# Optimization experiments

Measured on AMD Instinct MI355X. Metric: run time of the kernel, lower is better.

Reference implementation:

```python
import jax, jax.numpy as jnp
import numpy as np

D_MODEL = 1024
N_HEADS = 16
D_K = D_MODEL // N_HEADS  # 64
D_FF = 2688
THETA = 10000.0
EPS = 1e-5
B, S = 2, 2048


def _rmsnorm(x, w):
    xf = x.astype(jnp.float32)
    ms = jnp.mean(xf * xf, axis=-1, keepdims=True)
    return (xf * w * jax.lax.rsqrt(ms + EPS)).astype(x.dtype)


def _rope(x, cos, sin):
    # x: [B, S, H, D_K]; cos/sin: [S, D_K//2]
    xe = x[..., 0::2]
    xo = x[..., 1::2]
    c = cos[None, :, None, :]
    s = sin[None, :, None, :]
    re = xe * c - xo * s
    ro = xe * s + xo * c
    # interleave back to even/odd layout
    return jnp.stack([re, ro], axis=-1).reshape(x.shape)


def setup_inputs() -> dict:
    key = jax.random.key(0)
    ks = jax.random.split(key, 12)
    sc = 0.02  # keep activations numerically sane (stand-in for trunc_normal init)
    return {
        "x": jax.random.normal(ks[0], (B, S, D_MODEL), dtype=jnp.float32),
        "ln1_w": jax.random.normal(ks[1], (D_MODEL,), dtype=jnp.float32) * sc + 1.0,
        "q_w": jax.random.normal(ks[2], (D_MODEL, D_MODEL), dtype=jnp.float32) * sc,
        "k_w": jax.random.normal(ks[3], (D_MODEL, D_MODEL), dtype=jnp.float32) * sc,
        "v_w": jax.random.normal(ks[4], (D_MODEL, D_MODEL), dtype=jnp.float32) * sc,
        "o_w": jax.random.normal(ks[5], (D_MODEL, D_MODEL), dtype=jnp.float32) * sc,
        "ln2_w": jax.random.normal(ks[6], (D_MODEL,), dtype=jnp.float32) * sc + 1.0,
        "w1_w": jax.random.normal(ks[7], (D_FF, D_MODEL), dtype=jnp.float32) * sc,
        "w3_w": jax.random.normal(ks[8], (D_FF, D_MODEL), dtype=jnp.float32) * sc,
        "w2_w": jax.random.normal(ks[9], (D_MODEL, D_FF), dtype=jnp.float32) * sc,
        "token_positions": jnp.arange(S, dtype=jnp.int32),
    }


def reference(x, ln1_w, q_w, k_w, v_w, o_w, ln2_w, w1_w, w3_w, w2_w, token_positions):
    b, s, _ = x.shape
    # --- pre-norm attention sublayer ---
    h = _rmsnorm(x, ln1_w)
    Q = (h @ q_w.T).reshape(b, s, N_HEADS, D_K)
    K = (h @ k_w.T).reshape(b, s, N_HEADS, D_K)
    V = (h @ v_w.T).reshape(b, s, N_HEADS, D_K)

    # RoPE tables from token positions
    pos = token_positions.astype(jnp.float32)                      # [S]
    kk = jnp.arange(D_K // 2, dtype=jnp.float32)
    inv_freq = THETA ** (-2.0 * kk / D_K)                          # [D_K/2]
    ang = pos[:, None] * inv_freq[None, :]                          # [S, D_K/2]
    cos, sin = jnp.cos(ang), jnp.sin(ang)

    Qr = _rope(Q, cos, sin)
    Kr = _rope(K, cos, sin)

    scale = 1.0 / jnp.sqrt(jnp.float32(D_K))
    scores = jnp.einsum("bqhd,bkhd->bhqk", Qr, Kr) * scale          # [B,H,S,S]
    causal = jnp.tril(jnp.ones((s, s), dtype=bool))
    scores = jnp.where(causal[None, None], scores, jnp.float32(-10000.0))
    attn = jax.nn.softmax(scores, axis=-1)
    ctx = jnp.einsum("bhqk,bkhd->bqhd", attn, V).reshape(b, s, D_MODEL)
    x1 = x + ctx @ o_w.T

    # --- pre-norm SwiGLU FFN sublayer ---
    h2 = _rmsnorm(x1, ln2_w)
    g = h2 @ w1_w.T                                                 # [B,S,D_FF]
    u = h2 @ w3_w.T
    ffn = (g * jax.nn.sigmoid(g) * u) @ w2_w.T
    return x1 + ffn
```

## Files before the change

kernel.cpp:

```cpp
#include <hip/hip_runtime.h>
#include <cstdint>

#define DM   1024
#define NH   16
#define DK   64
#define DFF  2688
#define SEQ  2048
#define BB   2
#define MTOT (BB*SEQ)

typedef __attribute__((ext_vector_type(8))) short short8;
typedef __attribute__((ext_vector_type(4))) float f32x4;

typedef const __attribute__((address_space(1))) void* gaddr_t;
typedef __attribute__((address_space(3))) void* laddr_t;
#define GLOAD_LDS16(g, l) __builtin_amdgcn_global_load_lds((gaddr_t)(g), (laddr_t)(l), 16, 0, 0)
#define MFMA16(a, b, c) __builtin_amdgcn_mfma_f32_16x16x32_bf16((a), (b), (c), 0, 0, 0)
#define WAIT_LDS() __builtin_amdgcn_s_waitcnt(0xc07f)

__device__ __forceinline__ float bf2f(unsigned short u) {
    union { unsigned int i; float f; } v; v.i = ((unsigned int)u) << 16; return v.f;
}
__device__ __forceinline__ unsigned short f2bf(float f) {
    union { float f; unsigned int i; } v; v.f = f;
    unsigned int r = v.i + 0x7fffu + ((v.i >> 16) & 1u);
    return (unsigned short)(r >> 16);
}
__device__ __forceinline__ unsigned long long pack4bf(float a, float b, float c, float d) {
    return (unsigned long long)f2bf(a) | ((unsigned long long)f2bf(b) << 16)
         | ((unsigned long long)f2bf(c) << 32) | ((unsigned long long)f2bf(d) << 48);
}

__global__ __launch_bounds__(256)
void prep_k(const float* __restrict__ q_w, const float* __restrict__ k_w,
            const float* __restrict__ v_w, const float* __restrict__ o_w,
            const float* __restrict__ w1_w, const float* __restrict__ w3_w,
            const float* __restrict__ w2_w,
            unsigned short* __restrict__ Wqkv, unsigned short* __restrict__ Wo,
            unsigned short* __restrict__ W13, unsigned short* __restrict__ W2) {
    const int blk = blockIdx.x;
    const float* src; unsigned short* dst; int cols, rmul, roff, i;
    if (blk < 4096) {
        const int rr = blk >> 10;
        i = (blk & 1023) * 256 + threadIdx.x;
        cols = 1024; rmul = 1;
        if (rr == 0)      { src = q_w; dst = Wqkv; roff = 0; }
        else if (rr == 1) { src = k_w; dst = Wqkv; roff = 1024; }
        else if (rr == 2) { src = v_w; dst = Wqkv; roff = 2048; }
        else              { src = o_w; dst = Wo;   roff = 0; }
    } else if (blk < 6784) {
        i = (blk - 4096) * 256 + threadIdx.x; src = w1_w; dst = W13; cols = 1024; rmul = 2; roff = 0;
    } else if (blk < 9472) {
        i = (blk - 6784) * 256 + threadIdx.x; src = w3_w; dst = W13; cols = 1024; rmul = 2; roff = 1;
    } else {
        i = (blk - 9472) * 256 + threadIdx.x; src = w2_w; dst = W2;  cols = 2688; rmul = 1; roff = 0;
    }
    const int e = i * 4;
    const int r = e / cols, c = e - r * cols;
    const float4 v = *(const float4*)(src + e);
    ushort4 o;
    o.x = f2bf(v.x); o.y = f2bf(v.y); o.z = f2bf(v.z); o.w = f2bf(v.w);
    *(ushort4*)(dst + (size_t)(r * rmul + roff) * cols + c) = o;
}

__global__ __launch_bounds__(256)
void rmsnorm_k(const float* __restrict__ x, const float* __restrict__ w,
               unsigned short* __restrict__ out) {
    const int row = blockIdx.x;
    const int tid = threadIdx.x;
    const float4 v = ((const float4*)(x + (size_t)row * DM))[tid];
    float ss = v.x * v.x + v.y * v.y + v.z * v.z + v.w * v.w;
#pragma unroll
    for (int off = 32; off > 0; off >>= 1) ss += __shfl_down(ss, off, 64);
    __shared__ float sred[4];
    const int wave = tid >> 6, lane = tid & 63;
    if (lane == 0) sred[wave] = ss;
    __syncthreads();
    const float tot = sred[0] + sred[1] + sred[2] + sred[3];
    const float rinv = rsqrtf(tot * (1.0f / DM) + 1e-5f);
    const float4 wv = ((const float4*)w)[tid];
    ushort4 o;
    o.x = f2bf(v.x * wv.x * rinv);
    o.y = f2bf(v.y * wv.y * rinv);
    o.z = f2bf(v.z * wv.z * rinv);
    o.w = f2bf(v.w * wv.w * rinv);
    ((ushort4*)(out + (size_t)row * DM))[tid] = o;
}

__global__ void rope_tab_k(const int* __restrict__ pos, float* __restrict__ tab) {
    const int s = blockIdx.x, t = threadIdx.x;
    const int kk = t & 31;
    const float ang = (float)pos[s] * __expf(-0.28782313662f * (float)kk);
    tab[s * 64 + t] = (t < 32) ? cosf(ang) : sinf(ang);
}

template <int EPI>
__global__ __launch_bounds__(256)
void gemm128(const unsigned short* __restrict__ A,
             const unsigned short* __restrict__ B,
             unsigned short* __restrict__ O0,
             unsigned short* __restrict__ O1,
             unsigned short* __restrict__ O2,
             const float* __restrict__ ROPT,
             int N, int K) {
    __shared__ unsigned short As[4096];
    __shared__ unsigned short Bs[4096];
    const int tid = threadIdx.x;
    const int wave = tid >> 6, lane = tid & 63;
    const int l15 = lane & 15, quad = lane >> 4;
    const int m0 = blockIdx.y * 128, n0 = blockIdx.x * 128;
    const int wr = (wave >> 1) * 64, wc = (wave & 1) * 64;

    const f32x4 z4 = {0.f, 0.f, 0.f, 0.f};
    f32x4 acc[4][4];
#pragma unroll
    for (int i = 0; i < 4; i++)
#pragma unroll
        for (int j = 0; j < 4; j++) acc[i][j] = z4;

    const int c0 = tid, c1 = 256 + tid;
    const int k80 = c0 >> 7, mm0 = c0 & 127;
    const int k81 = c1 >> 7, mm1 = c1 & 127;
    const unsigned short* a0 = A + (size_t)(m0 + mm0) * K + k80 * 8;
    const unsigned short* a1 = A + (size_t)(m0 + mm1) * K + k81 * 8;
    const unsigned short* b0 = B + (size_t)(n0 + mm0) * K + k80 * 8;
    const unsigned short* b1 = B + (size_t)(n0 + mm1) * K + k81 * 8;
    unsigned short* lA0 = As + (wave * 64) * 8;
    unsigned short* lA1 = As + (256 + wave * 64) * 8;
    unsigned short* lB0 = Bs + (wave * 64) * 8;
    unsigned short* lB1 = Bs + (256 + wave * 64) * 8;

    for (int k0 = 0; k0 < K; k0 += 32) {
        __syncthreads();
        GLOAD_LDS16(a0 + k0, lA0);
        GLOAD_LDS16(a1 + k0, lA1);
        GLOAD_LDS16(b0 + k0, lB0);
        GLOAD_LDS16(b1 + k0, lB1);
        __syncthreads();
        short8 af[4], bg[4];
#pragma unroll
        for (int t = 0; t < 4; t++)
            af[t] = *(const short8*)(As + (quad * 128 + wr + t * 16 + l15) * 8);
#pragma unroll
        for (int t = 0; t < 4; t++)
            bg[t] = *(const short8*)(Bs + (quad * 128 + wc + t * 16 + l15) * 8);
#pragma unroll
        for (int i = 0; i < 4; i++)
#pragma unroll
            for (int j = 0; j < 4; j++)
                acc[i][j] = MFMA16(bg[j], af[i], acc[i][j]);
    }

#pragma unroll
    for (int i = 0; i < 4; i++) {
        const int r = m0 + wr + i * 16 + l15;
        if (EPI == 0) {
            const int b = r >> 11, s = r & (SEQ - 1);
            const float* rt = ROPT + s * 64;
#pragma unroll
            for (int j = 0; j < 4; j++) {
                const int cb = n0 + wc + j * 16;
                const int sec = cb >> 10;
                const int h = (cb & 1023) >> 6;
                const int cc0 = (cb & 63) + quad * 4;
                const f32x4 a = acc[i][j];
                if (sec < 2) {
                    const int p0 = cc0 >> 1;
                    const float cA = rt[p0],     sA = rt[32 + p0];
                    const float cB = rt[p0 + 1], sB = rt[32 + p0 + 1];
                    const float e0 = a[0] * cA - a[1] * sA;
                    const float o0 = a[0] * sA + a[1] * cA;
                    const float e1 = a[2] * cB - a[3] * sB;
                    const float o1 = a[2] * sB + a[3] * cB;
                    unsigned short* dst = (sec == 0) ? O0 : O1;
                    *(unsigned long long*)(dst + ((size_t)(b * NH + h) * SEQ + s) * DK + cc0) =
                        pack4bf(e0, o0, e1, o1);
                } else {
                    unsigned short* dst = O2 + ((size_t)(b * NH + h) * DK) * SEQ + s;
#pragma unroll
                    for (int t = 0; t < 4; t++)
                        dst[(size_t)(cc0 + t) * SEQ] = f2bf(a[t]);
                }
            }
        } else {
#pragma unroll
            for (int j = 0; j < 4; j++) {
                const int cc = n0 + wc + j * 16 + quad * 4;
                const f32x4 a = acc[i][j];
                const float s1 = a[0] * a[1] / (1.f + __expf(-a[0]));
                const float s2 = a[2] * a[3] / (1.f + __expf(-a[2]));
                *(unsigned int*)(O0 + (size_t)r * (DFF) + (cc >> 1)) =
                    (unsigned int)f2bf(s1) | ((unsigned int)f2bf(s2) << 16);
            }
        }
    }
}

__global__ __launch_bounds__(256, 4)
void gemm_thin(const unsigned short* __restrict__ A,
               const unsigned short* __restrict__ B,
               float* __restrict__ Cf,
               const float* __restrict__ R,
               int N, int K) {
    __shared__ unsigned short As[8192];
    __shared__ unsigned short Bs[4096];
    const int tid = threadIdx.x;
    const int wave = tid >> 6, lane = tid & 63;
    const int l15 = lane & 15, quad = lane >> 4;
    const int m0 = blockIdx.y * 128, n0 = blockIdx.x * 64;
    const int wr = (wave & 1) * 64, wc = (wave >> 1) * 32;

    const f32x4 z4 = {0.f, 0.f, 0.f, 0.f};
    f32x4 acc[4][2];
#pragma unroll
    for (int i = 0; i < 4; i++)
#pragma unroll
        for (int j = 0; j < 2; j++) acc[i][j] = z4;

    const unsigned short* ap[4];
    int al[4];
#pragma unroll
    for (int i = 0; i < 4; i++) {
        const int s = i * 256 + tid;
        ap[i] = A + (size_t)(m0 + (s & 127)) * K + (s >> 7) * 8;
        al[i] = (i * 256 + wave * 64) * 8;
    }
    const unsigned short* bp[2];
    int bl[2];
#pragma unroll
    for (int i = 0; i < 2; i++) {
        const int s = i * 256 + tid;
        bp[i] = B + (size_t)(n0 + (s & 63)) * K + (s >> 6) * 8;
        bl[i] = (i * 256 + wave * 64) * 8;
    }

    const int nk = K >> 6;
    for (int kc = 0; kc < nk; kc++) {
        __syncthreads();
#pragma unroll
        for (int i = 0; i < 4; i++) { GLOAD_LDS16(ap[i], &As[al[i]]); ap[i] += 64; }
#pragma unroll
        for (int i = 0; i < 2; i++) { GLOAD_LDS16(bp[i], &Bs[bl[i]]); bp[i] += 64; }
        __syncthreads();
#pragma unroll
        for (int h = 0; h < 2; h++) {
            short8 af[4], bg[2];
#pragma unroll
            for (int t = 0; t < 4; t++)
                af[t] = *(const short8*)(&As[((quad + 4 * h) * 128 + wr + t * 16 + l15) * 8]);
#pragma unroll
            for (int t = 0; t < 2; t++)
                bg[t] = *(const short8*)(&Bs[((quad + 4 * h) * 64 + wc + t * 16 + l15) * 8]);
#pragma unroll
            for (int i = 0; i < 4; i++)
#pragma unroll
                for (int j = 0; j < 2; j++)
                    acc[i][j] = MFMA16(bg[j], af[i], acc[i][j]);
        }
    }

#pragma unroll
    for (int i = 0; i < 4; i++) {
        const int r = m0 + wr + i * 16 + l15;
#pragma unroll
        for (int j = 0; j < 2; j++) {
            const int cc = n0 + wc + j * 16 + quad * 4;
            const size_t idx = (size_t)r * N + cc;
            const float4 rv = *(const float4*)(R + idx);
            float4 ov;
            ov.x = acc[i][j][0] + rv.x;
            ov.y = acc[i][j][1] + rv.y;
            ov.z = acc[i][j][2] + rv.z;
            ov.w = acc[i][j][3] + rv.w;
            *(float4*)(Cf + idx) = ov;
        }
    }
}

template <bool MASK>
__device__ __forceinline__ void softmax_tile(f32x4 st[4], float& li, unsigned short* Pw,
                                             int l15, int quad, int j0, int myq) {
    float lsum = 0.f;
#pragma unroll
    for (int t = 0; t < 4; t++) {
#pragma unroll
        for (int r = 0; r < 4; r++) {
            float v = st[t][r] * 0.125f;
            if (MASK) {
                const int key = j0 + t * 16 + quad * 4 + r;
                if (key > myq) v = -1e30f;
            }
            const float p = __expf(v);
            st[t][r] = p;
            lsum += p;
        }
        *(unsigned long long*)(Pw + l15 * 72 + t * 16 + quad * 4) =
            pack4bf(st[t][0], st[t][1], st[t][2], st[t][3]);
    }
    li += lsum;
}

__global__ __launch_bounds__(256, 2)
void attn_k(const unsigned short* __restrict__ Qr, const unsigned short* __restrict__ Kr,
            const unsigned short* __restrict__ Vt, unsigned short* __restrict__ ctx) {
    __shared__ unsigned short KVl[2][8192];
    __shared__ unsigned short Pl[4 * 2 * 1152];
    const int tid = threadIdx.x;
    const int wave = tid >> 6, lane = tid & 63;
    const int l15 = lane & 15, quad = lane >> 4;
    const int bh = blockIdx.y, b = bh >> 4, h = bh & 15;
    const int g = blockIdx.x;
    const int qtA = g * 4 + wave, qtB = 127 - qtA;
    const int q0A = qtA * 16, q0B = qtB * 16;
    const int countA = g + 1, countB = 32 - g;
    const unsigned short* Kb = Kr + (size_t)bh * SEQ * DK;
    const unsigned short* Vb = Vt + (size_t)bh * DK * SEQ;

    const unsigned short* QbA = Qr + ((size_t)bh * SEQ + q0A) * DK;
    const unsigned short* QbB = Qr + ((size_t)bh * SEQ + q0B) * DK;
    const short8 qfA0 = *(const short8*)(QbA + l15 * DK + quad * 8);
    const short8 qfA1 = *(const short8*)(QbA + l15 * DK + 32 + quad * 8);
    const short8 qfB0 = *(const short8*)(QbB + l15 * DK + quad * 8);
    const short8 qfB1 = *(const short8*)(QbB + l15 * DK + 32 + quad * 8);

    const int slot0 = wave * 128 + lane, slot1 = slot0 + 64;
    const int ck0 = slot0 >> 3, s0 = slot0 & 7;
    const int ck1 = slot1 >> 3, s1 = slot1 & 7;
    const unsigned short* kp0 = Kb + ck0 * 64 + (s0 ^ (ck0 & 7)) * 8;
    const unsigned short* kp1 = Kb + ck1 * 64 + (s1 ^ (ck1 & 7)) * 8;
    const unsigned short* vp0 = Vb + ck0 * 2048 + (s0 ^ (ck0 & 7)) * 8;
    const unsigned short* vp1 = Vb + ck1 * 2048 + (s1 ^ (ck1 & 7)) * 8;
    const int kb0 = wave * 1024, kb1 = kb0 + 512;

    unsigned short* PA = Pl + (wave * 2 + 0) * 1152;
    unsigned short* PB = Pl + (wave * 2 + 1) * 1152;

    const f32x4 z4 = {0.f, 0.f, 0.f, 0.f};
    f32x4 oA[4], oB[4];
#pragma unroll
    for (int d = 0; d < 4; d++) { oA[d] = z4; oB[d] = z4; }
    float liA = 0.f, liB = 0.f;
    const int myqA = q0A + l15, myqB = q0B + l15;
    const int xr = l15 & 7;

    GLOAD_LDS16(kp0, &KVl[0][kb0]);
    GLOAD_LDS16(kp1, &KVl[0][kb1]);
    GLOAD_LDS16(vp0, &KVl[0][4096 + kb0]);
    GLOAD_LDS16(vp1, &KVl[0][4096 + kb1]);
    kp0 += 4096; kp1 += 4096; vp0 += 64; vp1 += 64;

    for (int j = 0; j < countB; ++j) {
        const int bf = j & 1;
        const unsigned short* Kl = KVl[bf];
        const unsigned short* Vl = KVl[bf] + 4096;
        __syncthreads();
        if (j + 1 < countB) {
            GLOAD_LDS16(kp0, &KVl[bf ^ 1][kb0]);
            GLOAD_LDS16(kp1, &KVl[bf ^ 1][kb1]);
            GLOAD_LDS16(vp0, &KVl[bf ^ 1][4096 + kb0]);
            GLOAD_LDS16(vp1, &KVl[bf ^ 1][4096 + kb1]);
            kp0 += 4096; kp1 += 4096; vp0 += 64; vp1 += 64;
        }
        const int j0 = j * 64;
        short8 kf[4][2];
#pragma unroll
        for (int t = 0; t < 4; t++) {
            const unsigned short* kr = Kl + (t * 16 + l15) * 64;
            kf[t][0] = *(const short8*)(kr + (quad ^ xr) * 8);
            kf[t][1] = *(const short8*)(kr + ((4 + quad) ^ xr) * 8);
        }
        f32x4 stB[4];
#pragma unroll
        for (int t = 0; t < 4; t++)
            stB[t] = MFMA16(kf[t][1], qfB1, MFMA16(kf[t][0], qfB0, z4));
        const bool doA = (j < countA);
        if (doA) {
            f32x4 stA[4];
#pragma unroll
            for (int t = 0; t < 4; t++)
                stA[t] = MFMA16(kf[t][1], qfA1, MFMA16(kf[t][0], qfA0, z4));
            if (j == countA - 1) softmax_tile<true >(stA, liA, PA, l15, quad, j0, myqA);
            else                 softmax_tile<false>(stA, liA, PA, l15, quad, j0, myqA);
        }
        if (j == countB - 1) softmax_tile<true >(stB, liB, PB, l15, quad, j0, myqB);
        else                 softmax_tile<false>(stB, liB, PB, l15, quad, j0, myqB);
        WAIT_LDS();
        short8 vf[4][2];
#pragma unroll
        for (int dt = 0; dt < 4; dt++) {
            const unsigned short* vr = Vl + (dt * 16 + l15) * 64;
            vf[dt][0] = *(const short8*)(vr + (quad ^ xr) * 8);
            vf[dt][1] = *(const short8*)(vr + ((4 + quad) ^ xr) * 8);
        }
        {
            const short8 pfB0 = *(const short8*)(PB + l15 * 72 + quad * 8);
            const short8 pfB1 = *(const short8*)(PB + l15 * 72 + 32 + quad * 8);
#pragma unroll
            for (int dt = 0; dt < 4; dt++)
                oB[dt] = MFMA16(vf[dt][1], pfB1, MFMA16(vf[dt][0], pfB0, oB[dt]));
        }
        if (doA) {
            const short8 pfA0 = *(const short8*)(PA + l15 * 72 + quad * 8);
            const short8 pfA1 = *(const short8*)(PA + l15 * 72 + 32 + quad * 8);
#pragma unroll
            for (int dt = 0; dt < 4; dt++)
                oA[dt] = MFMA16(vf[dt][1], pfA1, MFMA16(vf[dt][0], pfA0, oA[dt]));
        }
    }
    liA += __shfl_xor(liA, 16, 64); liA += __shfl_xor(liA, 32, 64);
    liB += __shfl_xor(liB, 16, 64); liB += __shfl_xor(liB, 32, 64);
    const float invA = 1.0f / liA, invB = 1.0f / liB;
#pragma unroll
    for (int dt = 0; dt < 4; dt++) {
        *(unsigned long long*)(PA + l15 * 72 + dt * 16 + quad * 4) =
            pack4bf(oA[dt][0] * invA, oA[dt][1] * invA, oA[dt][2] * invA, oA[dt][3] * invA);
        *(unsigned long long*)(PB + l15 * 72 + dt * 16 + quad * 4) =
            pack4bf(oB[dt][0] * invB, oB[dt][1] * invB, oB[dt][2] * invB, oB[dt][3] * invB);
    }
    WAIT_LDS();
    const int row = lane >> 2, seg = (lane & 3) * 8;
#pragma unroll
    for (int p = 0; p < 2; p++) {
        const int cs = seg + p * 32;
        const uint4 va = *(const uint4*)(PA + row * 72 + cs);
        *(uint4*)(ctx + ((size_t)b * SEQ + q0A + row) * DM + h * DK + cs) = va;
        const uint4 vb = *(const uint4*)(PB + row * 72 + cs);
        *(uint4*)(ctx + ((size_t)b * SEQ + q0B + row) * DM + h * DK + cs) = vb;
    }
}

extern "C" void kernel_launch(void* const* d_in, const int* in_sizes, int n_in,
                              void* d_out, int out_size, void* d_ws, size_t ws_size,
                              hipStream_t stream) {
    const float* x     = (const float*)d_in[0];
    const float* ln1_w = (const float*)d_in[1];
    const float* q_w   = (const float*)d_in[2];
    const float* k_w   = (const float*)d_in[3];
    const float* v_w   = (const float*)d_in[4];
    const float* o_w   = (const float*)d_in[5];
    const float* ln2_w = (const float*)d_in[6];
    const float* w1_w  = (const float*)d_in[7];
    const float* w3_w  = (const float*)d_in[8];
    const float* w2_w  = (const float*)d_in[9];
    const int*   tpos  = (const int*)d_in[10];
    float* out = (float*)d_out;
    char* ws = (char*)d_ws;

    unsigned short* Wqkv = (unsigned short*)(ws + 0);
    unsigned short* Wo   = (unsigned short*)(ws + 6291456);
    unsigned short* W13  = (unsigned short*)(ws + 8388608);
    unsigned short* W2   = (unsigned short*)(ws + 19398656);
    float*          X1   = (float*)(ws + 24903680);
    float*          ROPT = (float*)(ws + 24903680);
    char* base = ws + 41680896;
    unsigned short* H    = (unsigned short*)(base);
    unsigned short* QR   = (unsigned short*)(base + 8388608);
    unsigned short* KR   = (unsigned short*)(base + 16777216);
    unsigned short* VT   = (unsigned short*)(base + 25165824);
    unsigned short* CTX  = (unsigned short*)(base + 33554432);
    unsigned short* H2   = (unsigned short*)(base);
    unsigned short* ACT  = (unsigned short*)(base + 41943040);

    prep_k<<<12160, 256, 0, stream>>>(q_w, k_w, v_w, o_w, w1_w, w3_w, w2_w,
                                      Wqkv, Wo, W13, W2);
    rope_tab_k<<<2048, 64, 0, stream>>>(tpos, ROPT);

    rmsnorm_k<<<4096, 256, 0, stream>>>(x, ln1_w, H);
    gemm128<0><<<dim3(24, 32), 256, 0, stream>>>(H, Wqkv, QR, KR, VT, ROPT, 3072, 1024);
    attn_k<<<dim3(16, 32), 256, 0, stream>>>(QR, KR, VT, CTX);
    gemm_thin<<<dim3(16, 32), 256, 0, stream>>>(CTX, Wo, X1, x, 1024, 1024);
    rmsnorm_k<<<4096, 256, 0, stream>>>(X1, ln2_w, H2);
    gemm128<1><<<dim3(42, 32), 256, 0, stream>>>(H2, W13, ACT, nullptr, nullptr, nullptr, 5376, 1024);
    gemm_thin<<<dim3(16, 32), 256, 0, stream>>>(ACT, W2, out, X1, 1024, 2688);
}
```

Baseline: 426.8 us.

## Double-buffer LDS tiles in gemm128 and gemm_thin to overlap loads with MFMA

Both GEMM kernels now keep two LDS buffers. The next K-slice is prefetched with global_load_lds while MFMAs run on the current buffer, and the loop drops to one barrier per iteration instead of two. This is meant to hide global-memory latency behind compute. In exchange LDS use doubles, and gemm_thin's launch bound falls from 4 to 2 blocks per CU, which may lower occupancy.

```diff
diff --git a/kernel.cpp b/kernel.cpp
--- a/kernel.cpp
+++ b/kernel.cpp
@@ -94,6 +94,22 @@
     tab[s * 64 + t] = (t < 32) ? cosf(ang) : sinf(ang);
 }
 
+#define G128_COMPUTE(BUF)                                                         \
+    do {                                                                          \
+        short8 af[4], bg[4];                                                      \
+        _Pragma("unroll")                                                         \
+        for (int t = 0; t < 4; t++)                                               \
+            af[t] = *(const short8*)(&As[BUF][(quad * 128 + wr + t * 16 + l15) * 8]); \
+        _Pragma("unroll")                                                         \
+        for (int t = 0; t < 4; t++)                                               \
+            bg[t] = *(const short8*)(&Bs[BUF][(quad * 128 + wc + t * 16 + l15) * 8]); \
+        _Pragma("unroll")                                                         \
+        for (int i = 0; i < 4; i++)                                               \
+            _Pragma("unroll")                                                     \
+            for (int j = 0; j < 4; j++)                                           \
+                acc[i][j] = MFMA16(bg[j], af[i], acc[i][j]);                      \
+    } while (0)
+
 template <int EPI>
 __global__ __launch_bounds__(256)
 void gemm128(const unsigned short* __restrict__ A,
@@ -103,8 +119,8 @@
              unsigned short* __restrict__ O2,
              const float* __restrict__ ROPT,
              int N, int K) {
-    __shared__ unsigned short As[4096];
-    __shared__ unsigned short Bs[4096];
+    __shared__ unsigned short As[2][4096];
+    __shared__ unsigned short Bs[2][4096];
     const int tid = threadIdx.x;
     const int wave = tid >> 6, lane = tid & 63;
     const int l15 = lane & 15, quad = lane >> 4;
@@ -125,31 +141,27 @@
     const unsigned short* a1 = A + (size_t)(m0 + mm1) * K + k81 * 8;
     const unsigned short* b0 = B + (size_t)(n0 + mm0) * K + k80 * 8;
     const unsigned short* b1 = B + (size_t)(n0 + mm1) * K + k81 * 8;
-    unsigned short* lA0 = As + (wave * 64) * 8;
-    unsigned short* lA1 = As + (256 + wave * 64) * 8;
-    unsigned short* lB0 = Bs + (wave * 64) * 8;
-    unsigned short* lB1 = Bs + (256 + wave * 64) * 8;
-
-    for (int k0 = 0; k0 < K; k0 += 32) {
+    const int oL0 = (wave * 64) * 8;
+    const int oL1 = (256 + wave * 64) * 8;
+
+    GLOAD_LDS16(a0, &As[0][oL0]);
+    GLOAD_LDS16(a1, &As[0][oL1]);
+    GLOAD_LDS16(b0, &Bs[0][oL0]);
+    GLOAD_LDS16(b1, &Bs[0][oL1]);
+    __syncthreads();
+
+    int cur = 0;
+    for (int k0 = 32; k0 < K; k0 += 32) {
+        const int nb = cur ^ 1;
+        GLOAD_LDS16(a0 + k0, &As[nb][oL0]);
+        GLOAD_LDS16(a1 + k0, &As[nb][oL1]);
+        GLOAD_LDS16(b0 + k0, &Bs[nb][oL0]);
+        GLOAD_LDS16(b1 + k0, &Bs[nb][oL1]);
+        G128_COMPUTE(cur);
         __syncthreads();
-        GLOAD_LDS16(a0 + k0, lA0);
-        GLOAD_LDS16(a1 + k0, lA1);
-        GLOAD_LDS16(b0 + k0, lB0);
-        GLOAD_LDS16(b1 + k0, lB1);
-        __syncthreads();
-        short8 af[4], bg[4];
-#pragma unroll
-        for (int t = 0; t < 4; t++)
-            af[t] = *(const short8*)(As + (quad * 128 + wr + t * 16 + l15) * 8);
-#pragma unroll
-        for (int t = 0; t < 4; t++)
-            bg[t] = *(const short8*)(Bs + (quad * 128 + wc + t * 16 + l15) * 8);
-#pragma unroll
-        for (int i = 0; i < 4; i++)
-#pragma unroll
-            for (int j = 0; j < 4; j++)
-                acc[i][j] = MFMA16(bg[j], af[i], acc[i][j]);
-    }
+        cur = nb;
+    }
+    G128_COMPUTE(cur);
 
 #pragma unroll
     for (int i = 0; i < 4; i++) {
@@ -196,14 +208,33 @@
     }
 }
 
-__global__ __launch_bounds__(256, 4)
+#define GT_COMPUTE(BUF)                                                           \
+    do {                                                                          \
+        _Pragma("unroll")                                                         \
+        for (int h = 0; h < 2; h++) {                                             \
+            short8 af[4], bg[2];                                                  \
+            _Pragma("unroll")                                                     \
+            for (int t = 0; t < 4; t++)                                           \
+                af[t] = *(const short8*)(&As[BUF][((quad + 4 * h) * 128 + wr + t * 16 + l15) * 8]); \
+            _Pragma("unroll")                                                     \
+            for (int t = 0; t < 2; t++)                                           \
+                bg[t] = *(const short8*)(&Bs[BUF][((quad + 4 * h) * 64 + wc + t * 16 + l15) * 8]); \
+            _Pragma("unroll")                                                     \
+            for (int i = 0; i < 4; i++)                                           \
+                _Pragma("unroll")                                                 \
+                for (int j = 0; j < 2; j++)                                       \
+                    acc[i][j] = MFMA16(bg[j], af[i], acc[i][j]);                  \
+        }                                                                         \
+    } while (0)
+
+__global__ __launch_bounds__(256, 2)
 void gemm_thin(const unsigned short* __restrict__ A,
                const unsigned short* __restrict__ B,
                float* __restrict__ Cf,
                const float* __restrict__ R,
                int N, int K) {
-    __shared__ unsigned short As[8192];
-    __shared__ unsigned short Bs[4096];
+    __shared__ unsigned short As[2][8192];
+    __shared__ unsigned short Bs[2][4096];
     const int tid = threadIdx.x;
     const int wave = tid >> 6, lane = tid & 63;
     const int l15 = lane & 15, quad = lane >> 4;
@@ -234,30 +265,25 @@
         bl[i] = (i * 256 + wave * 64) * 8;
     }
 
+#pragma unroll
+    for (int i = 0; i < 4; i++) { GLOAD_LDS16(ap[i], &As[0][al[i]]); ap[i] += 64; }
+#pragma unroll
+    for (int i = 0; i < 2; i++) { GLOAD_LDS16(bp[i], &Bs[0][bl[i]]); bp[i] += 64; }
+    __syncthreads();
+
+    int cur = 0;
     const int nk = K >> 6;
-    for (int kc = 0; kc < nk; kc++) {
+    for (int kc = 1; kc < nk; kc++) {
+        const int nb = cur ^ 1;
+#pragma unroll
+        for (int i = 0; i < 4; i++) { GLOAD_LDS16(ap[i], &As[nb][al[i]]); ap[i] += 64; }
+#pragma unroll
+        for (int i = 0; i < 2; i++) { GLOAD_LDS16(bp[i], &Bs[nb][bl[i]]); bp[i] += 64; }
+        GT_COMPUTE(cur);
         __syncthreads();
-#pragma unroll
-        for (int i = 0; i < 4; i++) { GLOAD_LDS16(ap[i], &As[al[i]]); ap[i] += 64; }
-#pragma unroll
-        for (int i = 0; i < 2; i++) { GLOAD_LDS16(bp[i], &Bs[bl[i]]); bp[i] += 64; }
-        __syncthreads();
-#pragma unroll
-        for (int h = 0; h < 2; h++) {
-            short8 af[4], bg[2];
-#pragma unroll
-            for (int t = 0; t < 4; t++)
-                af[t] = *(const short8*)(&As[((quad + 4 * h) * 128 + wr + t * 16 + l15) * 8]);
-#pragma unroll
-            for (int t = 0; t < 2; t++)
-                bg[t] = *(const short8*)(&Bs[((quad + 4 * h) * 64 + wc + t * 16 + l15) * 8]);
-#pragma unroll
-            for (int i = 0; i < 4; i++)
-#pragma unroll
-                for (int j = 0; j < 2; j++)
-                    acc[i][j] = MFMA16(bg[j], af[i], acc[i][j]);
-        }
-    }
+        cur = nb;
+    }
+    GT_COMPUTE(cur);
 
 #pragma unroll
     for (int i = 0; i < 4; i++) {
```

Measured after the change: 452.3 us. 1.06x slower.

## Triple-buffer LDS tiles in gemm128 with async prefetch two stages ahead

Applied to the files above, without the earlier changes.

Replaces the single-buffered load-sync-compute loop in the GEMM kernel with a three-stage LDS ring buffer. Global-to-LDS loads for tile t+2 are issued before computing tile t, and explicit vmcnt waits plus raw barriers replace __syncthreads. The goal is to hide global memory latency behind MFMA work. It triples LDS use per block (48KB), which can lower occupancy.

```diff
diff --git a/kernel.cpp b/kernel.cpp
--- a/kernel.cpp
+++ b/kernel.cpp
@@ -17,6 +17,12 @@
 #define GLOAD_LDS16(g, l) __builtin_amdgcn_global_load_lds((gaddr_t)(g), (laddr_t)(l), 16, 0, 0)
 #define MFMA16(a, b, c) __builtin_amdgcn_mfma_f32_16x16x32_bf16((a), (b), (c), 0, 0, 0)
 #define WAIT_LDS() __builtin_amdgcn_s_waitcnt(0xc07f)
+
+#define VMCNT(n) asm volatile("s_waitcnt vmcnt(" #n ")" ::: "memory")
+#define BAR() do { asm volatile("" ::: "memory"); \
+                   __builtin_amdgcn_s_barrier();  \
+                   asm volatile("" ::: "memory"); } while (0)
+#define SCHED_FENCE() __builtin_amdgcn_sched_barrier(0)
 
 __device__ __forceinline__ float bf2f(unsigned short u) {
     union { unsigned int i; float f; } v; v.i = ((unsigned int)u) << 16; return v.f;
@@ -103,8 +109,8 @@
              unsigned short* __restrict__ O2,
              const float* __restrict__ ROPT,
              int N, int K) {
-    __shared__ unsigned short As[4096];
-    __shared__ unsigned short Bs[4096];
+    __shared__ unsigned short As[3][4096];
+    __shared__ unsigned short Bs[3][4096];
     const int tid = threadIdx.x;
     const int wave = tid >> 6, lane = tid & 63;
     const int l15 = lane & 15, quad = lane >> 4;
@@ -125,30 +131,53 @@
     const unsigned short* a1 = A + (size_t)(m0 + mm1) * K + k81 * 8;
     const unsigned short* b0 = B + (size_t)(n0 + mm0) * K + k80 * 8;
     const unsigned short* b1 = B + (size_t)(n0 + mm1) * K + k81 * 8;
-    unsigned short* lA0 = As + (wave * 64) * 8;
-    unsigned short* lA1 = As + (256 + wave * 64) * 8;
-    unsigned short* lB0 = Bs + (wave * 64) * 8;
-    unsigned short* lB1 = Bs + (256 + wave * 64) * 8;
-
-    for (int k0 = 0; k0 < K; k0 += 32) {
-        __syncthreads();
-        GLOAD_LDS16(a0 + k0, lA0);
-        GLOAD_LDS16(a1 + k0, lA1);
-        GLOAD_LDS16(b0 + k0, lB0);
-        GLOAD_LDS16(b1 + k0, lB1);
-        __syncthreads();
-        short8 af[4], bg[4];
-#pragma unroll
-        for (int t = 0; t < 4; t++)
-            af[t] = *(const short8*)(As + (quad * 128 + wr + t * 16 + l15) * 8);
-#pragma unroll
-        for (int t = 0; t < 4; t++)
-            bg[t] = *(const short8*)(Bs + (quad * 128 + wc + t * 16 + l15) * 8);
-#pragma unroll
-        for (int i = 0; i < 4; i++)
-#pragma unroll
-            for (int j = 0; j < 4; j++)
-                acc[i][j] = MFMA16(bg[j], af[i], acc[i][j]);
+    const int oL0 = (wave * 64) * 8;
+    const int oL1 = (256 + wave * 64) * 8;
+
+    const int nt = K >> 5;
+
+    GLOAD_LDS16(a0, &As[0][oL0]);
+    GLOAD_LDS16(a1, &As[0][oL1]);
+    GLOAD_LDS16(b0, &Bs[0][oL0]);
+    GLOAD_LDS16(b1, &Bs[0][oL1]);
+    a0 += 32; a1 += 32; b0 += 32; b1 += 32;
+    GLOAD_LDS16(a0, &As[1][oL0]);
+    GLOAD_LDS16(a1, &As[1][oL1]);
+    GLOAD_LDS16(b0, &Bs[1][oL0]);
+    GLOAD_LDS16(b1, &Bs[1][oL1]);
+    a0 += 32; a1 += 32; b0 += 32; b1 += 32;
+
+    int bi = 0;
+    for (int t = 0; t < nt; ++t) {
+        if (t + 2 < nt) {
+            int pb = bi + 2; if (pb >= 3) pb -= 3;
+            GLOAD_LDS16(a0, &As[pb][oL0]);
+            GLOAD_LDS16(a1, &As[pb][oL1]);
+            GLOAD_LDS16(b0, &Bs[pb][oL0]);
+            GLOAD_LDS16(b1, &Bs[pb][oL1]);
+            a0 += 32; a1 += 32; b0 += 32; b1 += 32;
+            VMCNT(8);
+        } else {
+            VMCNT(0);
+        }
+        BAR();
+        SCHED_FENCE();
+        {
+            short8 af[4], bg[4];
+#pragma unroll
+            for (int tt = 0; tt < 4; tt++)
+                af[tt] = *(const short8*)(&As[bi][(quad * 128 + wr + tt * 16 + l15) * 8]);
+#pragma unroll
+            for (int tt = 0; tt < 4; tt++)
+                bg[tt] = *(const short8*)(&Bs[bi][(quad * 128 + wc + tt * 16 + l15) * 8]);
+#pragma unroll
+            for (int i = 0; i < 4; i++)
+#pragma unroll
+                for (int j = 0; j < 4; j++)
+                    acc[i][j] = MFMA16(bg[j], af[i], acc[i][j]);
+        }
+        BAR();
+        bi = (bi + 1 < 3) ? bi + 1 : 0;
     }
 
 #pragma unroll
```

New measurement: 436.4 us. +2.3%, slower.
